# Kernel tuning notes

Hardware: AMD Instinct MI355X
Metric: run time of the kernel (lower is better)

The kernel has to match this reference:

```python
import jax, jax.numpy as jnp
import numpy as np

ALPHA_1 = 1.0
ALPHA_2 = 1.0

def setup_inputs() -> dict:
    key = jax.random.key(0)
    k1, k2, k3, k4 = jax.random.split(key, 4)
    n, d = 4096, 1024
    # xavier_normal-ish scale for (d,d): std = sqrt(2/(d+d)) = 1/sqrt(d)
    s = 1.0 / np.sqrt(d)
    Y = jax.random.normal(k1, (n, d), dtype=jnp.float32)
    W = jax.random.normal(k2, (d, d), dtype=jnp.float32) * s
    Wf = jax.random.normal(k3, (d, d), dtype=jnp.float32) * s
    B = jax.random.normal(k4, (1, d), dtype=jnp.float32) * s
    return {"Y": Y, "W": W, "Wf": Wf, "B": B}

def reference(Y, W, Wf, B):
    # Attention: scores = Y @ (W^T W) @ Y^T = (Y W^T)(Y W^T)^T
    YWt = Y @ W.T                      # (n, d)
    A = jax.nn.softmax(YWt @ YWt.T, axis=-1)  # (n, n)
    Z = (1.0 - ALPHA_1) * Y + ALPHA_1 * (A @ Y)  # (n, d); alpha_1=1 -> A@Y
    # FFN: Wf_eff = -0.5*alpha_2*(Wf + Wf^T) + (1-alpha_2)*I; alpha_2=1
    d = Wf.shape[0]
    Wf_eff = -0.5 * ALPHA_2 * (Wf + Wf.T) + (1.0 - ALPHA_2) * jnp.eye(d, dtype=Wf.dtype)
    out = Z @ Wf_eff + B               # (n, d)
    out = jax.nn.relu(out)             # relu=True
    return out
```

## Files before the change

kernel.cpp:

```cpp
#include <hip/hip_runtime.h>
#include <cstdint>
#include <cmath>


typedef __attribute__((ext_vector_type(8))) short short8;
typedef __attribute__((ext_vector_type(4))) short short4v;
typedef __attribute__((ext_vector_type(4))) float f32x4;

__device__ __forceinline__ short f2bf(float x) {
    unsigned u = __builtin_bit_cast(unsigned, x);
    u += 0x7fffu + ((u >> 16) & 1u);
    return (short)(u >> 16);
}
__device__ __forceinline__ float bf2f(short s) {
    unsigned u = ((unsigned)(unsigned short)s) << 16;
    return __builtin_bit_cast(float, u);
}

typedef const __attribute__((address_space(1))) void* gas1_t;
typedef __attribute__((address_space(3))) void* las3_t;
__device__ __forceinline__ void cp16(const void* g, void* l) {
    __builtin_amdgcn_global_load_lds((gas1_t)(uintptr_t)g, (las3_t)(uintptr_t)l, 16, 0, 0);
}

template<bool SPLIT, int OUTMODE, bool SYMM>
__global__ __launch_bounds__(512, 4)
void mfma_gemm(const short* __restrict__ Ah, const short* __restrict__ Al,
               const short* __restrict__ Bh, const short* __restrict__ Bl,
               const float* __restrict__ bias, void* Co_, void* Cl_,
               int M, int N, int K)
{
    constexpr int BK = SPLIT ? 32 : 64;
    __shared__ short lds[2][16384];

    const int tid  = threadIdx.x;
    const int lane = tid & 63;
    const int wave = tid >> 6;
    const int wr   = wave >> 2;
    const int wc   = wave & 3;

    int bm, bn, bi = 0, bj = 0;
    if (SYMM) {
        const int NB = N >> 7;
        int lin = blockIdx.x;
        const int nwg = gridDim.x;
        if ((nwg & 7) == 0) lin = (lin & 7) * (nwg >> 3) + (lin >> 3);
        const float ff = (float)(2 * NB + 1);
        int i = (int)((ff - sqrtf(ff * ff - 8.0f * (float)lin)) * 0.5f);
        while ((i + 1) * (2 * NB - i) / 2 <= lin) ++i;
        while (i * (2 * NB - i + 1) / 2 > lin) --i;
        bi = i;
        bj = i + (lin - i * (2 * NB - i + 1) / 2);
        bm = bi << 7; bn = bj << 7;
    } else {
        const int gx  = gridDim.x;
        const int nwg = gx * gridDim.y;
        int lin = blockIdx.y * gx + blockIdx.x;
        if ((nwg & 7) == 0) { const int cpx = nwg >> 3; lin = (lin & 7) * cpx + (lin >> 3); }
        bm = (lin / gx) << 7;
        bn = (lin % gx) << 7;
    }

    f32x4 acc[4][2];
#pragma unroll
    for (int m = 0; m < 4; ++m)
#pragma unroll
        for (int n = 0; n < 2; ++n)
#pragma unroll
            for (int q = 0; q < 4; ++q) acc[m][n][q] = 0.f;

    const short *pA0, *pA1, *pB0, *pB1;
    if constexpr (SPLIT) {
        const int row = tid >> 2;
        const int csw = (tid & 3) ^ ((tid >> 3) & 3);
        const size_t oA = (size_t)(bm + row) * K + csw * 8;
        const size_t oB = (size_t)(bn + row) * K + csw * 8;
        pA0 = Ah + oA; pA1 = Al + oA;
        pB0 = Bh + oB; pB1 = Bl + oB;
    } else {
        const int row = tid >> 3;
        const int lch = (tid & 7) ^ ((tid >> 3) & 7);
        const size_t oA = (size_t)(bm + row) * K + lch * 8;
        const size_t oB = (size_t)(bn + row) * K + lch * 8;
        pA0 = Ah + oA; pA1 = pA0 + (size_t)64 * K;
        pB0 = Bh + oB; pB1 = pB0 + (size_t)64 * K;
    }

    auto stage = [&](int buf, int t) {
        short* db = &lds[buf][0] + tid * 8;
        const int ko = t * BK;
        cp16(pA0 + ko, db);
        cp16(pA1 + ko, db + 4096);
        cp16(pB0 + ko, db + 8192);
        cp16(pB1 + ko, db + 12288);
    };

    int aoff, boff;
    if constexpr (SPLIT) {
        const int swz = ((lane >> 4) ^ ((lane >> 1) & 3)) * 8;
        aoff = (wr * 64 + (lane & 15)) * 32 + swz;
        boff = (wc * 32 + (lane & 15)) * 32 + swz;
    } else {
        aoff = (wr * 64 + (lane & 15)) * 64;
        boff = (wc * 32 + (lane & 15)) * 64;
    }

    const int nt = K / BK;
    int cur = 0;

    stage(0, 0);
    asm volatile("s_waitcnt vmcnt(0)" ::: "memory");
    __syncthreads();

    for (int t = 0; t < nt; ++t) {
        if (t + 1 < nt) stage(cur ^ 1, t + 1);
        const short* base = &lds[cur][0];
        if constexpr (SPLIT) {
            short8 fah[4], fal[4];
#pragma unroll
            for (int m = 0; m < 4; ++m) {
                fah[m] = *(const short8*)(base + aoff + m * 512);
                fal[m] = *(const short8*)(base + 4096 + aoff + m * 512);
            }
#pragma unroll
            for (int n = 0; n < 2; ++n) {
                const short8 fbh = *(const short8*)(base + 8192 + boff + n * 512);
                const short8 fbl = *(const short8*)(base + 12288 + boff + n * 512);
#pragma unroll
                for (int m = 0; m < 4; ++m) {
                    acc[m][n] = __builtin_amdgcn_mfma_f32_16x16x32_bf16(fah[m], fbh, acc[m][n], 0, 0, 0);
                    acc[m][n] = __builtin_amdgcn_mfma_f32_16x16x32_bf16(fah[m], fbl, acc[m][n], 0, 0, 0);
                    acc[m][n] = __builtin_amdgcn_mfma_f32_16x16x32_bf16(fal[m], fbh, acc[m][n], 0, 0, 0);
                }
            }
        } else {
#pragma unroll
            for (int ks = 0; ks < 2; ++ks) {
                const int sw = ((ks * 4 + (lane >> 4)) ^ (lane & 7)) * 8;
                short8 fa[4], fb[2];
#pragma unroll
                for (int m = 0; m < 4; ++m)
                    fa[m] = *(const short8*)(base + aoff + sw + m * 1024);
#pragma unroll
                for (int n = 0; n < 2; ++n)
                    fb[n] = *(const short8*)(base + 8192 + boff + sw + n * 1024);
#pragma unroll
                for (int m = 0; m < 4; ++m)
#pragma unroll
                    for (int n = 0; n < 2; ++n)
                        acc[m][n] = __builtin_amdgcn_mfma_f32_16x16x32_bf16(fa[m], fb[n], acc[m][n], 0, 0, 0);
            }
        }
        asm volatile("s_waitcnt vmcnt(0)" ::: "memory");
        __syncthreads();
        cur ^= 1;
    }

    const int crow0 = bm + wr * 64 + ((lane >> 4) << 2);
    const int ccol0 = bn + wc * 32 + (lane & 15);
    if constexpr (OUTMODE == 2) {
        float* C = (float*)Co_;
#pragma unroll
        for (int n = 0; n < 2; ++n) {
            const int c = ccol0 + n * 16;
            const float bv = bias[c];
#pragma unroll
            for (int m = 0; m < 4; ++m)
#pragma unroll
                for (int q = 0; q < 4; ++q) {
                    const int r = crow0 + m * 16 + q;
                    C[(size_t)r * N + c] = fmaxf(acc[m][n][q] + bv, 0.f);
                }
        }
    } else if constexpr (OUTMODE == 1) {
        short* Ch = (short*)Co_;
#pragma unroll
        for (int n = 0; n < 2; ++n) {
            const int c = ccol0 + n * 16;
#pragma unroll
            for (int m = 0; m < 4; ++m)
#pragma unroll
                for (int q = 0; q < 4; ++q) {
                    const int r = crow0 + m * 16 + q;
                    Ch[(size_t)r * N + c] = f2bf(acc[m][n][q]);
                }
        }
    } else {
        short* Ch = (short*)Co_;
        short* Cl = (short*)Cl_;
        const bool mirror = SYMM && (bi != bj);
#pragma unroll
        for (int n = 0; n < 2; ++n) {
            const int c = ccol0 + n * 16;
#pragma unroll
            for (int m = 0; m < 4; ++m)
#pragma unroll
                for (int q = 0; q < 4; ++q) {
                    const int r = crow0 + m * 16 + q;
                    const float v = acc[m][n][q];
                    const short hh = f2bf(v);
                    const short ll = f2bf(v - bf2f(hh));
                    Ch[(size_t)r * N + c] = hh;
                    Cl[(size_t)r * N + c] = ll;
                    if (mirror) {
                        Ch[(size_t)c * N + r] = hh;
                        Cl[(size_t)c * N + r] = ll;
                    }
                }
        }
    }
}

__global__ __launch_bounds__(256)
void softmax_hi(short* __restrict__ Shi, const short* __restrict__ Slo)
{
    const int row = blockIdx.x;
    short8* ph = (short8*)(Shi + (size_t)row * 4096);
    const short8* pl = (const short8*)(Slo + (size_t)row * 4096);
    const int t = threadIdx.x;

    short8 h0 = ph[t], h1 = ph[t + 256];
    short8 l0 = pl[t], l1 = pl[t + 256];
    float x[16];
#pragma unroll
    for (int j = 0; j < 8; ++j) {
        x[j]     = bf2f(h0[j]) + bf2f(l0[j]);
        x[8 + j] = bf2f(h1[j]) + bf2f(l1[j]);
    }
    float mx = x[0];
#pragma unroll
    for (int j = 1; j < 16; ++j) mx = fmaxf(mx, x[j]);
#pragma unroll
    for (int off = 32; off > 0; off >>= 1) mx = fmaxf(mx, __shfl_xor(mx, off));

    __shared__ float rm[4], rs[4];
    const int wv = t >> 6, ln = t & 63;
    if (ln == 0) rm[wv] = mx;
    __syncthreads();
    mx = fmaxf(fmaxf(rm[0], rm[1]), fmaxf(rm[2], rm[3]));

    float s = 0.f;
#pragma unroll
    for (int j = 0; j < 16; ++j) { x[j] = __expf(x[j] - mx); s += x[j]; }
#pragma unroll
    for (int off = 32; off > 0; off >>= 1) s += __shfl_xor(s, off);
    if (ln == 0) rs[wv] = s;
    __syncthreads();
    s = rs[0] + rs[1] + rs[2] + rs[3];

    const float inv = 1.f / s;
    short8 o0, o1;
#pragma unroll
    for (int j = 0; j < 8; ++j) {
        o0[j] = f2bf(x[j] * inv);
        o1[j] = f2bf(x[8 + j] * inv);
    }
    ph[t] = o0; ph[t + 256] = o1;
}

__global__ __launch_bounds__(256)
void split_y(const float* __restrict__ Y, short* __restrict__ Yhi,
             short* __restrict__ Ylo, short* __restrict__ Yt)
{
    __shared__ float tb[64][65];
    const int rb = blockIdx.y * 64, cb = blockIdx.x * 64;
    const int t = threadIdx.x;
    const int r = t >> 4, c4 = (t & 15) * 4;
#pragma unroll
    for (int it = 0; it < 4; ++it) {
        const int row = rb + r + it * 16;
        const float4 v = *(const float4*)&Y[(size_t)row * 1024 + cb + c4];
        const float f[4] = {v.x, v.y, v.z, v.w};
        short4v h, l;
#pragma unroll
        for (int k = 0; k < 4; ++k) {
            const short hh = f2bf(f[k]);
            h[k] = hh;
            l[k] = f2bf(f[k] - bf2f(hh));
        }
        *(short4v*)&Yhi[(size_t)row * 1024 + cb + c4] = h;
        *(short4v*)&Ylo[(size_t)row * 1024 + cb + c4] = l;
        tb[r + it * 16][c4 + 0] = v.x; tb[r + it * 16][c4 + 1] = v.y;
        tb[r + it * 16][c4 + 2] = v.z; tb[r + it * 16][c4 + 3] = v.w;
    }
    __syncthreads();
    const int orow = t >> 2, oc0 = (t & 3) * 16;
    short8 h8[2];
#pragma unroll
    for (int g = 0; g < 2; ++g)
#pragma unroll
        for (int j = 0; j < 8; ++j)
            h8[g][j] = f2bf(tb[oc0 + g * 8 + j][orow]);
    const size_t ob = (size_t)(cb + orow) * 4096 + rb + oc0;
    *(short8*)&Yt[ob] = h8[0];
    *(short8*)&Yt[ob + 8] = h8[1];
}

__global__ __launch_bounds__(256)
void split_w(const float* __restrict__ Wm, short* __restrict__ Wh, short* __restrict__ Wl)
{
    const size_t idx = ((size_t)blockIdx.x * 256 + threadIdx.x) * 4;
    const float4 v = *(const float4*)&Wm[idx];
    const float f[4] = {v.x, v.y, v.z, v.w};
    short4v h, l;
#pragma unroll
    for (int k = 0; k < 4; ++k) {
        const short hh = f2bf(f[k]);
        h[k] = hh;
        l[k] = f2bf(f[k] - bf2f(hh));
    }
    *(short4v*)&Wh[idx] = h;
    *(short4v*)&Wl[idx] = l;
}

__global__ __launch_bounds__(256)
void symm_hi(const float* __restrict__ Wf, short* __restrict__ Fh)
{
    const int i  = blockIdx.x;
    const int j0 = threadIdx.x * 4;
    const float4 rv = *(const float4*)&Wf[(size_t)i * 1024 + j0];
    const float c0 = Wf[(size_t)(j0 + 0) * 1024 + i];
    const float c1 = Wf[(size_t)(j0 + 1) * 1024 + i];
    const float c2 = Wf[(size_t)(j0 + 2) * 1024 + i];
    const float c3 = Wf[(size_t)(j0 + 3) * 1024 + i];
    short4v h;
    h[0] = f2bf(-0.5f * (rv.x + c0));
    h[1] = f2bf(-0.5f * (rv.y + c1));
    h[2] = f2bf(-0.5f * (rv.z + c2));
    h[3] = f2bf(-0.5f * (rv.w + c3));
    *(short4v*)&Fh[(size_t)i * 1024 + j0] = h;
}

extern "C" void kernel_launch(void* const* d_in, const int* in_sizes, int n_in,
                              void* d_out, int out_size, void* d_ws, size_t ws_size,
                              hipStream_t stream)
{
    const float* Y  = (const float*)d_in[0];
    const float* W  = (const float*)d_in[1];
    const float* Wf = (const float*)d_in[2];
    const float* Bb = (const float*)d_in[3];
    float* out = (float*)d_out;

    const int n = 4096, d = 1024;

    char* w = (char*)d_ws;
    short* Ythi = (short*)w; w += (size_t)d * n * 2;
    short* Wfeh = (short*)w; w += (size_t)d * d * 2;
    short* YWth = (short*)w; w += (size_t)n * d * 2;
    short* YWtl = (short*)w; w += (size_t)n * d * 2;
    short* Shi  = (short*)w; w += (size_t)n * n * 2;
    short* Slo  = (short*)w; w += (size_t)n * n * 2;
    short* Yhi = Shi;
    short* Ylo = Yhi + (size_t)n * d;
    short* Whi = Ylo + (size_t)n * d;
    short* Wlo = Whi + (size_t)d * d;
    short* Zhi = YWth;

    split_y<<<dim3(16, 64), 256, 0, stream>>>(Y, Yhi, Ylo, Ythi);
    split_w<<<dim3(1024), 256, 0, stream>>>(W, Whi, Wlo);
    symm_hi<<<dim3(1024), 256, 0, stream>>>(Wf, Wfeh);

    mfma_gemm<true, 0, false><<<dim3(8, 32), 512, 0, stream>>>(
        Yhi, Ylo, Whi, Wlo, nullptr, YWth, YWtl, n, d, d);

    mfma_gemm<true, 0, true><<<dim3(528), 512, 0, stream>>>(
        YWth, YWtl, YWth, YWtl, nullptr, Shi, Slo, n, n, d);

    softmax_hi<<<dim3(n), 256, 0, stream>>>(Shi, Slo);

    mfma_gemm<false, 1, false><<<dim3(8, 32), 512, 0, stream>>>(
        Shi, nullptr, Ythi, nullptr, nullptr, Zhi, nullptr, n, d, n);

    mfma_gemm<false, 2, false><<<dim3(8, 32), 512, 0, stream>>>(
        Zhi, nullptr, Wfeh, nullptr, Bb, out, nullptr, n, d, d);
}
```

Measured before the change: 306.2 us.

## Deepen GEMM K-loop to four-stage LDS pipeline with partial vmcnt waits

Replaces the double-buffered K-loop with a four-buffer ring that keeps three tile loads in flight. It waits with partial vmcnt counts and uses a single barrier per iteration instead of a full drain plus syncthreads. It also loads all fragments before issuing the MFMAs, wrapped in s_setprio to favour matrix issue. The aim is to hide global-to-LDS latency behind compute. In exchange LDS per block doubles to 128KB and launch bounds drop to 2, which cuts resident blocks per CU and may reduce latency hiding across blocks.

Result: no change. 300.4 us (-1.9%).

```diff
diff --git a/kernel.cpp b/kernel.cpp
--- a/kernel.cpp
+++ b/kernel.cpp
@@ -24,14 +24,14 @@
 }
 
 template<bool SPLIT, int OUTMODE, bool SYMM>
-__global__ __launch_bounds__(512, 4)
+__global__ __launch_bounds__(512, 2)
 void mfma_gemm(const short* __restrict__ Ah, const short* __restrict__ Al,
                const short* __restrict__ Bh, const short* __restrict__ Bl,
                const float* __restrict__ bias, void* Co_, void* Cl_,
                int M, int N, int K)
 {
     constexpr int BK = SPLIT ? 32 : 64;
-    __shared__ short lds[2][16384];
+    __shared__ short lds[4][16384];
 
     const int tid  = threadIdx.x;
     const int lane = tid & 63;
@@ -86,8 +86,8 @@
         pB0 = Bh + oB; pB1 = pB0 + (size_t)64 * K;
     }
 
-    auto stage = [&](int buf, int t) {
-        short* db = &lds[buf][0] + tid * 8;
+    auto stage = [&](int t) {
+        short* db = &lds[t & 3][0] + tid * 8;
         const int ko = t * BK;
         cp16(pA0 + ko, db);
         cp16(pA1 + ko, db + 4096);
@@ -106,17 +106,25 @@
     }
 
     const int nt = K / BK;
-    int cur = 0;
-
-    stage(0, 0);
-    asm volatile("s_waitcnt vmcnt(0)" ::: "memory");
-    __syncthreads();
+
+    stage(0); stage(1); stage(2);
 
     for (int t = 0; t < nt; ++t) {
-        if (t + 1 < nt) stage(cur ^ 1, t + 1);
-        const short* base = &lds[cur][0];
+        if (t < nt - 2) {
+            asm volatile("s_waitcnt vmcnt(8)" ::: "memory");
+        } else if (t == nt - 2) {
+            asm volatile("s_waitcnt vmcnt(4)" ::: "memory");
+        } else {
+            asm volatile("s_waitcnt vmcnt(0)" ::: "memory");
+        }
+        __builtin_amdgcn_s_barrier();
+        __builtin_amdgcn_sched_barrier(0);
+
+        if (t + 3 < nt) stage(t + 3);
+
+        const short* base = &lds[t & 3][0];
         if constexpr (SPLIT) {
-            short8 fah[4], fal[4];
+            short8 fah[4], fal[4], fbh[2], fbl[2];
 #pragma unroll
             for (int m = 0; m < 4; ++m) {
                 fah[m] = *(const short8*)(base + aoff + m * 512);
@@ -124,36 +132,41 @@
             }
 #pragma unroll
             for (int n = 0; n < 2; ++n) {
-                const short8 fbh = *(const short8*)(base + 8192 + boff + n * 512);
-                const short8 fbl = *(const short8*)(base + 12288 + boff + n * 512);
-#pragma unroll
-                for (int m = 0; m < 4; ++m) {
-                    acc[m][n] = __builtin_amdgcn_mfma_f32_16x16x32_bf16(fah[m], fbh, acc[m][n], 0, 0, 0);
-                    acc[m][n] = __builtin_amdgcn_mfma_f32_16x16x32_bf16(fah[m], fbl, acc[m][n], 0, 0, 0);
-                    acc[m][n] = __builtin_amdgcn_mfma_f32_16x16x32_bf16(fal[m], fbh, acc[m][n], 0, 0, 0);
+                fbh[n] = *(const short8*)(base + 8192 + boff + n * 512);
+                fbl[n] = *(const short8*)(base + 12288 + boff + n * 512);
+            }
+            __builtin_amdgcn_s_setprio(1);
+#pragma unroll
+            for (int m = 0; m < 4; ++m)
+#pragma unroll
+                for (int n = 0; n < 2; ++n) {
+                    acc[m][n] = __builtin_amdgcn_mfma_f32_16x16x32_bf16(fah[m], fbh[n], acc[m][n], 0, 0, 0);
+                    acc[m][n] = __builtin_amdgcn_mfma_f32_16x16x32_bf16(fah[m], fbl[n], acc[m][n], 0, 0, 0);
+                    acc[m][n] = __builtin_amdgcn_mfma_f32_16x16x32_bf16(fal[m], fbh[n], acc[m][n], 0, 0, 0);
                 }
-            }
+            __builtin_amdgcn_s_setprio(0);
         } else {
+            short8 fa[2][4], fb[2][2];
 #pragma unroll
             for (int ks = 0; ks < 2; ++ks) {
                 const int sw = ((ks * 4 + (lane >> 4)) ^ (lane & 7)) * 8;
-                short8 fa[4], fb[2];
 #pragma unroll
                 for (int m = 0; m < 4; ++m)
-                    fa[m] = *(const short8*)(base + aoff + sw + m * 1024);
+                    fa[ks][m] = *(const short8*)(base + aoff + sw + m * 1024);
 #pragma unroll
                 for (int n = 0; n < 2; ++n)
-                    fb[n] = *(const short8*)(base + 8192 + boff + sw + n * 1024);
+                    fb[ks][n] = *(const short8*)(base + 8192 + boff + sw + n * 1024);
+            }
+            __builtin_amdgcn_s_setprio(1);
+#pragma unroll
+            for (int ks = 0; ks < 2; ++ks)
 #pragma unroll
                 for (int m = 0; m < 4; ++m)
 #pragma unroll
                     for (int n = 0; n < 2; ++n)
-                        acc[m][n] = __builtin_amdgcn_mfma_f32_16x16x32_bf16(fa[m], fb[n], acc[m][n], 0, 0, 0);
-            }
-        }
-        asm volatile("s_waitcnt vmcnt(0)" ::: "memory");
-        __syncthreads();
-        cur ^= 1;
+                        acc[m][n] = __builtin_amdgcn_mfma_f32_16x16x32_bf16(fa[ks][m], fb[ks][n], acc[m][n], 0, 0, 0);
+            __builtin_amdgcn_s_setprio(0);
+        }
     }
 
     const int crow0 = bm + wr * 64 + ((lane >> 4) << 2);
```
